# Kernel optimization log

Measured on AMD Instinct MI355X. Metric: run time of the kernel, lower is better.

The kernel has to match this reference:

```python
import jax, jax.numpy as jnp
import numpy as np

N, H = 65536, 256
RHO_REF = 1000.0
MOMENTUM_W, CONTINUITY_W = 1.0, 10.0


def setup_inputs() -> dict:
    key = jax.random.key(0)
    ks = jax.random.split(key, 6)
    sc = lambda k, shape, fan_in: jax.random.normal(k, shape, jnp.float32) * (1.0 / fan_in) ** 0.5
    return {
        "sample_points": jax.random.normal(ks[0], (N, 3), jnp.float32),
        "sample_times": jax.random.uniform(ks[1], (N, 1), jnp.float32),
        "viscosity": jax.random.uniform(ks[2], (N,), jnp.float32) * 1e-3 + 1e-6,
        "W1": sc(ks[3], (4, H), 4),
        "b1": jnp.zeros((H,), jnp.float32),
        "W2": sc(ks[4], (H, H), H),
        "b2": jnp.zeros((H,), jnp.float32),
        "W3": sc(ks[5], (H, 5), H),
        "b3": jnp.zeros((5,), jnp.float32),
    }


def reference(sample_points, sample_times, viscosity, W1, b1, W2, b2, W3, b3):
    gravity = jnp.array([0.0, -9.81, 0.0], dtype=sample_points.dtype)

    def mlp(z):  # z: (4,) = (x, y, zcoord, t) -> (5,) = (ux, uy, uz, p, rho_raw)
        h = jnp.tanh(z @ W1 + b1)
        h = jnp.tanh(h @ W2 + b2)
        return h @ W3 + b3

    def up_fn(z):  # (ux, uy, uz, p)
        return mlp(z)[:4]

    def u_fn(z):  # (ux, uy, uz)
        return mlp(z)[:3]

    def per_point(z):
        out = mlp(z)
        u = out[:3]
        rho = RHO_REF * (1.0 + 0.1 * jnp.tanh(out[4]))
        J = jax.jacfwd(up_fn)(z)                      # (4,4): d[u,p]/d[x,y,z,t]
        Hs = jax.jacfwd(jax.jacfwd(u_fn))(z)          # (3,4,4): second derivs of u
        lap = Hs[:, 0, 0] + Hs[:, 1, 1] + Hs[:, 2, 2]  # (3,) spatial Laplacian of u
        return u, rho, J, lap

    z = jnp.concatenate([sample_points, sample_times], axis=1)  # (N,4)
    u, rho, J, lap = jax.vmap(per_point)(z)

    du_dt = J[:, :3, 3]                                # (N,3)
    conv = jnp.einsum('nj,nij->ni', u, J[:, :3, :3])   # (u . grad) u
    grad_p = J[:, 3, :3]                               # (N,3)
    R = du_dt + conv + grad_p / rho[:, None] - viscosity[:, None] * lap - gravity[None, :]
    R_cont = J[:, 0, 0] + J[:, 1, 1] + J[:, 2, 2]      # div u

    momentum_loss = (R ** 2).mean(axis=0).sum()
    continuity_loss = (R_cont ** 2).mean()
    total = MOMENTUM_W * momentum_loss + CONTINUITY_W * continuity_loss
    return jnp.stack([total, momentum_loss, continuity_loss])
```

## Files before the change

kernel.cpp:

```cpp
#include <hip/hip_runtime.h>


#define NPTS 65536
#define TPB  8
#define NBLOCKS 256
#define TILES 32
#define KPAD 264
#define W3T_OFF 135168
#define PART_OFF 143360
#define TSZ 32768

typedef short s16x8 __attribute__((ext_vector_type(8)));
typedef float f32x4 __attribute__((ext_vector_type(4)));

static __device__ __forceinline__ unsigned short f2bf(float f){
  unsigned int u = __float_as_uint(f);
  u = (u + 0x7FFFu + ((u >> 16) & 1u)) >> 16;
  return (unsigned short)u;
}
static __device__ __forceinline__ unsigned cvtpk_bf16(float lo, float hi){
  unsigned r;
  asm("v_cvt_pk_bf16_f32 %0, %1, %2" : "=v"(r) : "v"(lo), "v"(hi));
  return r;
}
static __device__ __forceinline__ float fast_tanh(float x){
  float e = __builtin_amdgcn_exp2f(x * 2.8853900817779268f);
  return 1.f - 2.f * __builtin_amdgcn_rcpf(e + 1.f);
}

__global__ void prep_w2t(const float* __restrict__ W2, unsigned short* __restrict__ w2t){
  int k = blockIdx.x, j = threadIdx.x;
  w2t[j * KPAD + k] = f2bf(W2[k * 256 + j]);
}
__global__ void prep_w3t(const float* __restrict__ W3, unsigned short* __restrict__ w3t){
  int idx = blockIdx.x * 256 + threadIdx.x;
  int n = idx >> 8, k = idx & 255;
  w3t[n * 256 + k] = (n < 5) ? f2bf(W3[k * 5 + n]) : (unsigned short)0;
}

__launch_bounds__(512, 2)
__global__ void ns_main(const float* __restrict__ pts, const float* __restrict__ times,
                        const float* __restrict__ visc,
                        const float* __restrict__ W1, const float* __restrict__ b1,
                        const float* __restrict__ b2, const float* __restrict__ b3,
                        const unsigned short* __restrict__ w2t,
                        const unsigned short* __restrict__ w3t,
                        float* __restrict__ parts){
  __shared__ __align__(16) unsigned char sA[3 * TSZ];

  const int t   = threadIdx.x;
  const int blk = blockIdx.x;
  const int wid = t >> 6, lane = t & 63;
  const int g = lane >> 4, r16 = lane & 15;
  const int wr = wid >> 2, wc = wid & 3;
  const int xorv = (r16 & 7) << 4;

  const int p8 = t >> 6;
  const int jo = (t & 63) << 2;
  const float4 wa  = *(const float4*)(W1 + jo);
  const float4 wb  = *(const float4*)(W1 + 256 + jo);
  const float4 wc4 = *(const float4*)(W1 + 512 + jo);
  const float4 wd  = *(const float4*)(W1 + 768 + jo);
  const float4 bb  = *(const float4*)(b1 + jo);

  const unsigned char* w2tB = (const unsigned char*)w2t;
  const unsigned char* bp0 = w2tB + (((wc*64 +  0 + r16)*KPAD + g*8) << 1);
  const unsigned char* bp1 = w2tB + (((wc*64 + 16 + r16)*KPAD + g*8) << 1);
  const unsigned char* bp2 = w2tB + (((wc*64 + 32 + r16)*KPAD + g*8) << 1);
  const unsigned char* bp3 = w2tB + (((wc*64 + 48 + r16)*KPAD + g*8) << 1);
  float b2c[4];
  #pragma unroll
  for (int nt = 0; nt < 4; ++nt) b2c[nt] = b2[wc*64 + nt*16 + r16];
  const unsigned char* w3tB = (const unsigned char*)w3t + ((r16*256 + g*8) << 1);
  const float b3v = (r16 < 5) ? b3[r16] : 0.f;

  const int w3i = wid & 3;
  const int ptL = 2*w3i + ((r16 >> 2) & 1);
  const int jrow = ((ptL & 4) << 3) + ((ptL & 3) << 2) + (r16 & 3) + ((r16 >> 3) << 4);
  const int g3off = jrow * 512;
  const int g3sw  = (jrow & 7) << 4;

  float accM = 0.f, accC = 0.f;

  unsigned char *jA = sA, *jB = sA + TSZ, *jC = sA + 2*TSZ;

#define L1_TILE(NBASE, BASE) do {                                               \
    int n_ = (NBASE) + p8;                                                      \
    float z0_ = pts[n_*3+0], z1_ = pts[n_*3+1], z2_ = pts[n_*3+2], z3_ = times[n_]; \
    float th_[4], sg_[4], m2_[4];                                               \
    _Pragma("unroll")                                                           \
    for (int jj = 0; jj < 4; ++jj){                                             \
      float a_ = (&bb.x)[jj] + z0_*(&wa.x)[jj] + z1_*(&wb.x)[jj]                \
                             + z2_*(&wc4.x)[jj] + z3_*(&wd.x)[jj];              \
      float h_ = fast_tanh(a_);                                                 \
      th_[jj] = h_; sg_[jj] = 1.f - h_*h_; m2_[jj] = -2.f*h_*sg_[jj];           \
    }                                                                           \
    _Pragma("unroll")                                                           \
    for (int c = 0; c < 8; ++c){                                                \
      float x_[4];                                                              \
      _Pragma("unroll")                                                         \
      for (int jj = 0; jj < 4; ++jj){                                           \
        float w0_ = (&wa.x)[jj], w1_ = (&wb.x)[jj], w2_ = (&wc4.x)[jj];         \
        float v_;                                                               \
        if      (c == 0) v_ = th_[jj];                                          \
        else if (c == 1) v_ = sg_[jj]*w0_;                                      \
        else if (c == 2) v_ = sg_[jj]*w1_;                                      \
        else if (c == 3) v_ = sg_[jj]*w2_;                                      \
        else if (c == 4) v_ = sg_[jj]*(&wd.x)[jj];                              \
        else if (c == 5) v_ = m2_[jj]*w0_*w0_;                                  \
        else if (c == 6) v_ = m2_[jj]*w1_*w1_;                                  \
        else             v_ = m2_[jj]*w2_*w2_;                                  \
        x_[jj] = v_;                                                            \
      }                                                                         \
      int row_ = ((p8 & 4) << 3) + ((c & 4) << 2) + ((p8 & 3) << 2) + (c & 3);  \
      int off_ = row_*512 + (((jo << 1)) ^ ((row_ & 7) << 4));                  \
      uint2 v2_; v2_.x = cvtpk_bf16(x_[0], x_[1]); v2_.y = cvtpk_bf16(x_[2], x_[3]); \
      *(uint2*)((BASE) + off_) = v2_;                                           \
    }                                                                           \
  } while (0)

#define GEMM2_TILE(BASE, ACC) do {                                              \
    int abase_ = (wr*32 + r16)*512;                                             \
    s16x8 bc0_ = *(const s16x8*)(bp0), bc1_ = *(const s16x8*)(bp1);             \
    s16x8 bc2_ = *(const s16x8*)(bp2), bc3_ = *(const s16x8*)(bp3);             \
    _Pragma("unroll")                                                           \
    for (int ks = 0; ks < 8; ++ks){                                             \
      int X_ = ((ks*64) + (g << 4)) ^ xorv;                                     \
      s16x8 a0_ = *(const s16x8*)((BASE) + abase_ + X_);                        \
      s16x8 a1_ = *(const s16x8*)((BASE) + abase_ + 8192 + X_);                 \
      s16x8 bn0_, bn1_, bn2_, bn3_;                                             \
      if (ks < 7){                                                              \
        bn0_ = *(const s16x8*)(bp0 + (ks+1)*64);                                \
        bn1_ = *(const s16x8*)(bp1 + (ks+1)*64);                                \
        bn2_ = *(const s16x8*)(bp2 + (ks+1)*64);                                \
        bn3_ = *(const s16x8*)(bp3 + (ks+1)*64);                                \
      }                                                                         \
      __builtin_amdgcn_s_setprio(1);                                            \
      ACC[0][0] = __builtin_amdgcn_mfma_f32_16x16x32_bf16(a0_, bc0_, ACC[0][0], 0, 0, 0); \
      ACC[1][0] = __builtin_amdgcn_mfma_f32_16x16x32_bf16(a1_, bc0_, ACC[1][0], 0, 0, 0); \
      ACC[0][1] = __builtin_amdgcn_mfma_f32_16x16x32_bf16(a0_, bc1_, ACC[0][1], 0, 0, 0); \
      ACC[1][1] = __builtin_amdgcn_mfma_f32_16x16x32_bf16(a1_, bc1_, ACC[1][1], 0, 0, 0); \
      ACC[0][2] = __builtin_amdgcn_mfma_f32_16x16x32_bf16(a0_, bc2_, ACC[0][2], 0, 0, 0); \
      ACC[1][2] = __builtin_amdgcn_mfma_f32_16x16x32_bf16(a1_, bc2_, ACC[1][2], 0, 0, 0); \
      ACC[0][3] = __builtin_amdgcn_mfma_f32_16x16x32_bf16(a0_, bc3_, ACC[0][3], 0, 0, 0); \
      ACC[1][3] = __builtin_amdgcn_mfma_f32_16x16x32_bf16(a1_, bc3_, ACC[1][3], 0, 0, 0); \
      __builtin_amdgcn_s_setprio(0);                                            \
      bc0_ = bn0_; bc1_ = bn1_; bc2_ = bn2_; bc3_ = bn3_;                       \
    }                                                                           \
  } while (0)

#define RC_TILE(BASE, ACC) do {                                                 \
    _Pragma("unroll")                                                           \
    for (int nt = 0; nt < 4; ++nt){                                             \
      f32x4 v_ = ACC[0][nt];              \
      f32x4 w_ = ACC[1][nt];              \
      float gv_ = fast_tanh(v_[0] + b2c[nt]);                                   \
      float s2_ = 1.f - gv_*gv_;                                                \
      float t2_ = -2.f * gv_ * s2_;                                             \
      float r0_ = gv_,       r1_ = s2_*v_[1], r2_ = s2_*v_[2], r3_ = s2_*v_[3]; \
      float r4_ = s2_*w_[0];                                                    \
      float r5_ = fmaf(t2_*v_[1], v_[1], s2_*w_[1]);                            \
      float r6_ = fmaf(t2_*v_[2], v_[2], s2_*w_[2]);                            \
      float r7_ = fmaf(t2_*v_[3], v_[3], s2_*w_[3]);                            \
      int colb_ = (wc*64 + nt*16 + r16) << 1;                                   \
      int rb_   = (wr*32 + g*4)*512;                                            \
      unsigned u_;                                                              \
      u_ = cvtpk_bf16(r0_, r4_);                                                \
      *(unsigned short*)((BASE) + rb_        + (colb_ ^ ((((g&1)<<2)+0) << 4)))        = (unsigned short)u_; \
      *(unsigned short*)((BASE) + rb_        + (colb_ ^ ((((g&1)<<2)+0) << 4)) + 8192) = (unsigned short)(u_ >> 16); \
      u_ = cvtpk_bf16(r1_, r5_);                                                \
      *(unsigned short*)((BASE) + rb_ + 512  + (colb_ ^ ((((g&1)<<2)+1) << 4)))        = (unsigned short)u_; \
      *(unsigned short*)((BASE) + rb_ + 512  + (colb_ ^ ((((g&1)<<2)+1) << 4)) + 8192) = (unsigned short)(u_ >> 16); \
      u_ = cvtpk_bf16(r2_, r6_);                                                \
      *(unsigned short*)((BASE) + rb_ + 1024 + (colb_ ^ ((((g&1)<<2)+2) << 4)))        = (unsigned short)u_; \
      *(unsigned short*)((BASE) + rb_ + 1024 + (colb_ ^ ((((g&1)<<2)+2) << 4)) + 8192) = (unsigned short)(u_ >> 16); \
      u_ = cvtpk_bf16(r3_, r7_);                                                \
      *(unsigned short*)((BASE) + rb_ + 1536 + (colb_ ^ ((((g&1)<<2)+3) << 4)))        = (unsigned short)u_; \
      *(unsigned short*)((BASE) + rb_ + 1536 + (colb_ ^ ((((g&1)<<2)+3) << 4)) + 8192) = (unsigned short)(u_ >> 16); \
    }                                                                           \
  } while (0)

#define GEMM3_TAIL(BASE, NBASE) do {                                            \
    f32x4 a3_ = (f32x4){0.f, 0.f, 0.f, 0.f};                                    \
    _Pragma("unroll")                                                           \
    for (int ks = 0; ks < 8; ++ks){                                             \
      int X_ = ((ks*64) + (g << 4)) ^ g3sw;                                     \
      s16x8 av_ = *(const s16x8*)((BASE) + g3off + X_);                         \
      s16x8 bv_ = *(const s16x8*)(w3tB + ks*64);                                \
      a3_ = __builtin_amdgcn_mfma_f32_16x16x32_bf16(av_, bv_, a3_, 0, 0, 0);    \
    }                                                                           \
    float o4_ = __shfl_xor(a3_[0], 32, 64);                                     \
    float o5_ = __shfl_xor(a3_[1], 32, 64);                                     \
    float o6_ = __shfl_xor(a3_[2], 32, 64);                                     \
    float o7_ = __shfl_xor(a3_[3], 32, 64);                                     \
    float o0_ = a3_[0] + b3v, o1_ = a3_[1], o2_ = a3_[2], o3_ = a3_[3];         \
    int sl_ = lane & 16;                                                        \
    float u0_ = __shfl(o0_, sl_ | 0, 64);                                       \
    float u1_ = __shfl(o0_, sl_ | 1, 64);                                       \
    float u2_ = __shfl(o0_, sl_ | 2, 64);                                       \
    float rhoA_ = __shfl(o0_, sl_ | 4, 64);                                     \
    float gpx_ = __shfl(o1_, sl_ | 3, 64);                                      \
    float gpy_ = __shfl(o2_, sl_ | 3, 64);                                      \
    float gpz_ = __shfl(o3_, sl_ | 3, 64);                                      \
    float c00_ = __shfl(o1_, sl_ | 0, 64);                                      \
    float c11_ = __shfl(o2_, sl_ | 1, 64);                                      \
    float c22_ = __shfl(o3_, sl_ | 2, 64);                                      \
    float rho_ = 1000.f * (1.f + 0.1f * fast_tanh(rhoA_));                      \
    float rr_  = __builtin_amdgcn_rcpf(rho_);                                   \
    float vis_ = visc[(NBASE) + ptL];                                           \
    float lap_ = o5_ + o6_ + o7_;                                               \
    float cv_  = u0_*o1_ + u1_*o2_ + u2_*o3_;                                   \
    float gp_  = (r16 == 0) ? gpx_ : ((r16 == 1) ? gpy_ : gpz_);                \
    float R_   = o4_ + cv_ + gp_*rr_ - vis_*lap_ + ((r16 == 1) ? 9.81f : 0.f);  \
    if (lane < 32){                                                             \
      if (r16 < 3) accM += R_*R_;                                               \
      else if (r16 == 3){ float Rc_ = c00_ + c11_ + c22_; accC += Rc_*Rc_; }    \
    }                                                                           \
  } while (0)

  L1_TILE(blk*TILES*TPB, jA);
  __syncthreads();

  for (int i = 0; i < TILES; ++i){
    f32x4 acc[2][4];
    #pragma unroll
    for (int a = 0; a < 2; ++a)
      #pragma unroll
      for (int b = 0; b < 4; ++b)
        acc[a][b] = (f32x4){0.f, 0.f, 0.f, 0.f};
    GEMM2_TILE(jA, acc);
    if (i < TILES-1) L1_TILE((blk*TILES + i + 1)*TPB, jB);
    __syncthreads();

    RC_TILE(jA, acc);
    if (i > 0 && wid >= 4) GEMM3_TAIL(jC, (blk*TILES + i - 1)*TPB);
    __syncthreads();

    unsigned char* tmp = jA; jA = jB; jB = jC; jC = tmp;
  }
  if (wid >= 4) GEMM3_TAIL(jC, (blk*TILES + TILES - 1)*TPB);

  #pragma unroll
  for (int off = 1; off < 64; off <<= 1){
    accM += __shfl_xor(accM, off, 64);
    accC += __shfl_xor(accC, off, 64);
  }
  __syncthreads();
  float* red = (float*)sA;
  if (lane == 0){ red[wid*2] = accM; red[wid*2+1] = accC; }
  __syncthreads();
  if (t == 0){
    float m = 0.f, c = 0.f;
    #pragma unroll
    for (int w = 0; w < 8; ++w){ m += red[w*2]; c += red[w*2+1]; }
    float2 pr; pr.x = m; pr.y = c;
    *(float2*)(parts + blk*2) = pr;
  }
#undef L1_TILE
#undef GEMM2_TILE
#undef RC_TILE
#undef GEMM3_TAIL
}

__global__ void ns_reduce(const float* __restrict__ parts, float* __restrict__ out){
  int t = threadIdx.x;
  float a = 0.f, b = 0.f;
  if (t < NBLOCKS){ a = parts[2*t]; b = parts[2*t + 1]; }
  #pragma unroll
  for (int off = 32; off; off >>= 1){
    a += __shfl_down(a, off, 64);
    b += __shfl_down(b, off, 64);
  }
  __shared__ float sa[4], sb[4];
  int wid = t >> 6, lane = t & 63;
  if (lane == 0){ sa[wid] = a; sb[wid] = b; }
  __syncthreads();
  if (t == 0){
    float A = sa[0] + sa[1] + sa[2] + sa[3];
    float B = sb[0] + sb[1] + sb[2] + sb[3];
    float mom  = A / (float)NPTS;
    float cont = B / (float)NPTS;
    out[0] = mom + 10.f * cont;
    out[1] = mom;
    out[2] = cont;
  }
}

extern "C" void kernel_launch(void* const* d_in, const int* in_sizes, int n_in,
                              void* d_out, int out_size, void* d_ws, size_t ws_size,
                              hipStream_t stream) {
  const float* pts   = (const float*)d_in[0];
  const float* times = (const float*)d_in[1];
  const float* visc  = (const float*)d_in[2];
  const float* W1    = (const float*)d_in[3];
  const float* b1    = (const float*)d_in[4];
  const float* W2    = (const float*)d_in[5];
  const float* b2    = (const float*)d_in[6];
  const float* W3    = (const float*)d_in[7];
  const float* b3    = (const float*)d_in[8];
  float* out = (float*)d_out;

  unsigned short* w2t = (unsigned short*)d_ws;
  unsigned short* w3t = (unsigned short*)((char*)d_ws + W3T_OFF);
  float* parts        = (float*)((char*)d_ws + PART_OFF);

  prep_w2t<<<256, 256, 0, stream>>>(W2, w2t);
  prep_w3t<<<16, 256, 0, stream>>>(W3, w3t);
  ns_main<<<NBLOCKS, 512, 0, stream>>>(pts, times, visc, W1, b1, b2, b3, w2t, w3t, parts);
  ns_reduce<<<1, 256, 0, stream>>>(parts, out);
}
```

Measured before the change: 129.8 us.

## Split block into two staggered wave groups ping-ponging over separate LDS tiles

The 8 waves are split into two groups of 4. Each group owns its own pair of LDS tile buffers (LDS grows from 3 to 4 tiles) and processes alternate tiles. The groups run offset by one phase, so one group's MFMA GEMM2 overlaps the other's layer-1, tanh epilogue and GEMM3 work. Each wave now computes a full 64x64 output block (4x4 MFMA accumulators), and the B-fragment register prefetch is dropped. This trades more registers and LDS, plus two extra loop steps, for better overlap of matrix-core and vector work within a block.

After: 163.7 us. 26.1% more time.

```diff
diff --git a/kernel.cpp b/kernel.cpp
--- a/kernel.cpp
+++ b/kernel.cpp
@@ -46,17 +46,16 @@
                         const unsigned short* __restrict__ w2t,
                         const unsigned short* __restrict__ w3t,
                         float* __restrict__ parts){
-  __shared__ __align__(16) unsigned char sA[3 * TSZ];
+  __shared__ __align__(16) unsigned char sA[4 * TSZ];
 
   const int t   = threadIdx.x;
   const int blk = blockIdx.x;
   const int wid = t >> 6, lane = t & 63;
+  const int grp = wid >> 2, q = wid & 3;
   const int g = lane >> 4, r16 = lane & 15;
-  const int wr = wid >> 2, wc = wid & 3;
   const int xorv = (r16 & 7) << 4;
-
-  const int p8 = t >> 6;
-  const int jo = (t & 63) << 2;
+  const int jo = lane << 2;
+
   const float4 wa  = *(const float4*)(W1 + jo);
   const float4 wb  = *(const float4*)(W1 + 256 + jo);
   const float4 wc4 = *(const float4*)(W1 + 512 + jo);
@@ -64,123 +63,139 @@
   const float4 bb  = *(const float4*)(b1 + jo);
 
   const unsigned char* w2tB = (const unsigned char*)w2t;
-  const unsigned char* bp0 = w2tB + (((wc*64 +  0 + r16)*KPAD + g*8) << 1);
-  const unsigned char* bp1 = w2tB + (((wc*64 + 16 + r16)*KPAD + g*8) << 1);
-  const unsigned char* bp2 = w2tB + (((wc*64 + 32 + r16)*KPAD + g*8) << 1);
-  const unsigned char* bp3 = w2tB + (((wc*64 + 48 + r16)*KPAD + g*8) << 1);
+  const unsigned char* bp0 = w2tB + (((q*64 +  0 + r16)*KPAD + g*8) << 1);
+  const unsigned char* bp1 = w2tB + (((q*64 + 16 + r16)*KPAD + g*8) << 1);
+  const unsigned char* bp2 = w2tB + (((q*64 + 32 + r16)*KPAD + g*8) << 1);
+  const unsigned char* bp3 = w2tB + (((q*64 + 48 + r16)*KPAD + g*8) << 1);
   float b2c[4];
   #pragma unroll
-  for (int nt = 0; nt < 4; ++nt) b2c[nt] = b2[wc*64 + nt*16 + r16];
+  for (int nt = 0; nt < 4; ++nt) b2c[nt] = b2[q*64 + nt*16 + r16];
   const unsigned char* w3tB = (const unsigned char*)w3t + ((r16*256 + g*8) << 1);
   const float b3v = (r16 < 5) ? b3[r16] : 0.f;
 
-  const int w3i = wid & 3;
-  const int ptL = 2*w3i + ((r16 >> 2) & 1);
+  const int ptL  = 2*q + ((r16 >> 2) & 1);
   const int jrow = ((ptL & 4) << 3) + ((ptL & 3) << 2) + (r16 & 3) + ((r16 >> 3) << 4);
   const int g3off = jrow * 512;
   const int g3sw  = (jrow & 7) << 4;
 
+  const int tbase = blk * (TILES * TPB);
+
   float accM = 0.f, accC = 0.f;
-
-  unsigned char *jA = sA, *jB = sA + TSZ, *jC = sA + 2*TSZ;
-
-#define L1_TILE(NBASE, BASE) do {                                               \
-    int n_ = (NBASE) + p8;                                                      \
-    float z0_ = pts[n_*3+0], z1_ = pts[n_*3+1], z2_ = pts[n_*3+2], z3_ = times[n_]; \
-    float th_[4], sg_[4], m2_[4];                                               \
-    _Pragma("unroll")                                                           \
-    for (int jj = 0; jj < 4; ++jj){                                             \
-      float a_ = (&bb.x)[jj] + z0_*(&wa.x)[jj] + z1_*(&wb.x)[jj]                \
-                             + z2_*(&wc4.x)[jj] + z3_*(&wd.x)[jj];              \
-      float h_ = fast_tanh(a_);                                                 \
-      th_[jj] = h_; sg_[jj] = 1.f - h_*h_; m2_[jj] = -2.f*h_*sg_[jj];           \
-    }                                                                           \
-    _Pragma("unroll")                                                           \
-    for (int c = 0; c < 8; ++c){                                                \
-      float x_[4];                                                              \
+  f32x4 acc[4][4];
+
+#define L1_T(NBASE, BASE) do {                                                  \
+    _Pragma("unroll")                                                           \
+    for (int pp = 0; pp < 2; ++pp){                                             \
+      int p_ = 2*q + pp;                                                        \
+      int n_ = (NBASE) + p_;                                                    \
+      float z0_ = pts[n_*3+0], z1_ = pts[n_*3+1], z2_ = pts[n_*3+2], z3_ = times[n_]; \
+      float th_[4], sg_[4], m2_[4];                                             \
       _Pragma("unroll")                                                         \
       for (int jj = 0; jj < 4; ++jj){                                           \
-        float w0_ = (&wa.x)[jj], w1_ = (&wb.x)[jj], w2_ = (&wc4.x)[jj];         \
-        float v_;                                                               \
-        if      (c == 0) v_ = th_[jj];                                          \
-        else if (c == 1) v_ = sg_[jj]*w0_;                                      \
-        else if (c == 2) v_ = sg_[jj]*w1_;                                      \
-        else if (c == 3) v_ = sg_[jj]*w2_;                                      \
-        else if (c == 4) v_ = sg_[jj]*(&wd.x)[jj];                              \
-        else if (c == 5) v_ = m2_[jj]*w0_*w0_;                                  \
-        else if (c == 6) v_ = m2_[jj]*w1_*w1_;                                  \
-        else             v_ = m2_[jj]*w2_*w2_;                                  \
-        x_[jj] = v_;                                                            \
+        float a_ = (&bb.x)[jj] + z0_*(&wa.x)[jj] + z1_*(&wb.x)[jj]              \
+                               + z2_*(&wc4.x)[jj] + z3_*(&wd.x)[jj];            \
+        float h_ = fast_tanh(a_);                                               \
+        th_[jj] = h_; sg_[jj] = 1.f - h_*h_; m2_[jj] = -2.f*h_*sg_[jj];         \
       }                                                                         \
-      int row_ = ((p8 & 4) << 3) + ((c & 4) << 2) + ((p8 & 3) << 2) + (c & 3);  \
-      int off_ = row_*512 + (((jo << 1)) ^ ((row_ & 7) << 4));                  \
-      uint2 v2_; v2_.x = cvtpk_bf16(x_[0], x_[1]); v2_.y = cvtpk_bf16(x_[2], x_[3]); \
-      *(uint2*)((BASE) + off_) = v2_;                                           \
+      _Pragma("unroll")                                                         \
+      for (int c = 0; c < 8; ++c){                                              \
+        float x_[4];                                                            \
+        _Pragma("unroll")                                                       \
+        for (int jj = 0; jj < 4; ++jj){                                         \
+          float w0_ = (&wa.x)[jj], w1_ = (&wb.x)[jj], w2_ = (&wc4.x)[jj];       \
+          float v_;                                                             \
+          if      (c == 0) v_ = th_[jj];                                        \
+          else if (c == 1) v_ = sg_[jj]*w0_;                                    \
+          else if (c == 2) v_ = sg_[jj]*w1_;                                    \
+          else if (c == 3) v_ = sg_[jj]*w2_;                                    \
+          else if (c == 4) v_ = sg_[jj]*(&wd.x)[jj];                            \
+          else if (c == 5) v_ = m2_[jj]*w0_*w0_;                                \
+          else if (c == 6) v_ = m2_[jj]*w1_*w1_;                                \
+          else             v_ = m2_[jj]*w2_*w2_;                                \
+          x_[jj] = v_;                                                          \
+        }                                                                       \
+        int row_ = ((p_ & 4) << 3) + ((c & 4) << 2) + ((p_ & 3) << 2) + (c & 3);\
+        int off_ = row_*512 + ((jo << 1) ^ ((row_ & 7) << 4));                  \
+        uint2 v2_; v2_.x = cvtpk_bf16(x_[0], x_[1]); v2_.y = cvtpk_bf16(x_[2], x_[3]); \
+        *(uint2*)((BASE) + off_) = v2_;                                         \
+      }                                                                         \
     }                                                                           \
   } while (0)
 
-#define GEMM2_TILE(BASE, ACC) do {                                              \
-    int abase_ = (wr*32 + r16)*512;                                             \
-    s16x8 bc0_ = *(const s16x8*)(bp0), bc1_ = *(const s16x8*)(bp1);             \
-    s16x8 bc2_ = *(const s16x8*)(bp2), bc3_ = *(const s16x8*)(bp3);             \
+#define G2_T(BASE) do {                                                         \
+    _Pragma("unroll")                                                           \
+    for (int a_ = 0; a_ < 4; ++a_)                                              \
+      _Pragma("unroll")                                                         \
+      for (int b_ = 0; b_ < 4; ++b_)                                            \
+        acc[a_][b_] = (f32x4){0.f, 0.f, 0.f, 0.f};                              \
+    int abase_ = r16*512;                                                       \
     _Pragma("unroll")                                                           \
     for (int ks = 0; ks < 8; ++ks){                                             \
       int X_ = ((ks*64) + (g << 4)) ^ xorv;                                     \
-      s16x8 a0_ = *(const s16x8*)((BASE) + abase_ + X_);                        \
-      s16x8 a1_ = *(const s16x8*)((BASE) + abase_ + 8192 + X_);                 \
-      s16x8 bn0_, bn1_, bn2_, bn3_;                                             \
-      if (ks < 7){                                                              \
-        bn0_ = *(const s16x8*)(bp0 + (ks+1)*64);                                \
-        bn1_ = *(const s16x8*)(bp1 + (ks+1)*64);                                \
-        bn2_ = *(const s16x8*)(bp2 + (ks+1)*64);                                \
-        bn3_ = *(const s16x8*)(bp3 + (ks+1)*64);                                \
+      s16x8 af0_ = *(const s16x8*)((BASE) + abase_ + X_);                       \
+      s16x8 af1_ = *(const s16x8*)((BASE) + abase_ +  8192 + X_);               \
+      s16x8 af2_ = *(const s16x8*)((BASE) + abase_ + 16384 + X_);               \
+      s16x8 af3_ = *(const s16x8*)((BASE) + abase_ + 24576 + X_);               \
+      s16x8 b0_ = *(const s16x8*)(bp0 + ks*64);                                 \
+      s16x8 b1_ = *(const s16x8*)(bp1 + ks*64);                                 \
+      s16x8 b2_ = *(const s16x8*)(bp2 + ks*64);                                 \
+      s16x8 b3_ = *(const s16x8*)(bp3 + ks*64);                                 \
+      __builtin_amdgcn_s_setprio(1);                                            \
+      acc[0][0] = __builtin_amdgcn_mfma_f32_16x16x32_bf16(af0_, b0_, acc[0][0], 0, 0, 0); \
+      acc[1][0] = __builtin_amdgcn_mfma_f32_16x16x32_bf16(af1_, b0_, acc[1][0], 0, 0, 0); \
+      acc[2][0] = __builtin_amdgcn_mfma_f32_16x16x32_bf16(af2_, b0_, acc[2][0], 0, 0, 0); \
+      acc[3][0] = __builtin_amdgcn_mfma_f32_16x16x32_bf16(af3_, b0_, acc[3][0], 0, 0, 0); \
+      acc[0][1] = __builtin_amdgcn_mfma_f32_16x16x32_bf16(af0_, b1_, acc[0][1], 0, 0, 0); \
+      acc[1][1] = __builtin_amdgcn_mfma_f32_16x16x32_bf16(af1_, b1_, acc[1][1], 0, 0, 0); \
+      acc[2][1] = __builtin_amdgcn_mfma_f32_16x16x32_bf16(af2_, b1_, acc[2][1], 0, 0, 0); \
+      acc[3][1] = __builtin_amdgcn_mfma_f32_16x16x32_bf16(af3_, b1_, acc[3][1], 0, 0, 0); \
+      acc[0][2] = __builtin_amdgcn_mfma_f32_16x16x32_bf16(af0_, b2_, acc[0][2], 0, 0, 0); \
+      acc[1][2] = __builtin_amdgcn_mfma_f32_16x16x32_bf16(af1_, b2_, acc[1][2], 0, 0, 0); \
+      acc[2][2] = __builtin_amdgcn_mfma_f32_16x16x32_bf16(af2_, b2_, acc[2][2], 0, 0, 0); \
+      acc[3][2] = __builtin_amdgcn_mfma_f32_16x16x32_bf16(af3_, b2_, acc[3][2], 0, 0, 0); \
+      acc[0][3] = __builtin_amdgcn_mfma_f32_16x16x32_bf16(af0_, b3_, acc[0][3], 0, 0, 0); \
+      acc[1][3] = __builtin_amdgcn_mfma_f32_16x16x32_bf16(af1_, b3_, acc[1][3], 0, 0, 0); \
+      acc[2][3] = __builtin_amdgcn_mfma_f32_16x16x32_bf16(af2_, b3_, acc[2][3], 0, 0, 0); \
+      acc[3][3] = __builtin_amdgcn_mfma_f32_16x16x32_bf16(af3_, b3_, acc[3][3], 0, 0, 0); \
+      __builtin_amdgcn_s_setprio(0);                                            \
+    }                                                                           \
+  } while (0)
+
+#define RC_T(BASE) do {                                                         \
+    _Pragma("unroll")                                                           \
+    for (int pr = 0; pr < 2; ++pr){                                             \
+      _Pragma("unroll")                                                         \
+      for (int nt = 0; nt < 4; ++nt){                                           \
+        f32x4 v_ = acc[2*pr][nt];                                               \
+        f32x4 w_ = acc[2*pr+1][nt];                                             \
+        float gv_ = fast_tanh(v_[0] + b2c[nt]);                                 \
+        float s2_ = 1.f - gv_*gv_;                                              \
+        float t2_ = -2.f * gv_ * s2_;                                           \
+        float r0_ = gv_,       r1_ = s2_*v_[1], r2_ = s2_*v_[2], r3_ = s2_*v_[3]; \
+        float r4_ = s2_*w_[0];                                                  \
+        float r5_ = fmaf(t2_*v_[1], v_[1], s2_*w_[1]);                          \
+        float r6_ = fmaf(t2_*v_[2], v_[2], s2_*w_[2]);                          \
+        float r7_ = fmaf(t2_*v_[3], v_[3], s2_*w_[3]);                          \
+        int colb_ = (q*64 + nt*16 + r16) << 1;                                  \
+        int rb_   = pr*16384 + (g*4)*512;                                       \
+        unsigned u_;                                                            \
+        u_ = cvtpk_bf16(r0_, r4_);                                              \
+        *(unsigned short*)((BASE) + rb_        + (colb_ ^ ((((g&1)<<2)+0) << 4)))        = (unsigned short)u_; \
+        *(unsigned short*)((BASE) + rb_        + (colb_ ^ ((((g&1)<<2)+0) << 4)) + 8192) = (unsigned short)(u_ >> 16); \
+        u_ = cvtpk_bf16(r1_, r5_);                                              \
+        *(unsigned short*)((BASE) + rb_ + 512  + (colb_ ^ ((((g&1)<<2)+1) << 4)))        = (unsigned short)u_; \
+        *(unsigned short*)((BASE) + rb_ + 512  + (colb_ ^ ((((g&1)<<2)+1) << 4)) + 8192) = (unsigned short)(u_ >> 16); \
+        u_ = cvtpk_bf16(r2_, r6_);                                              \
+        *(unsigned short*)((BASE) + rb_ + 1024 + (colb_ ^ ((((g&1)<<2)+2) << 4)))        = (unsigned short)u_; \
+        *(unsigned short*)((BASE) + rb_ + 1024 + (colb_ ^ ((((g&1)<<2)+2) << 4)) + 8192) = (unsigned short)(u_ >> 16); \
+        u_ = cvtpk_bf16(r3_, r7_);                                              \
+        *(unsigned short*)((BASE) + rb_ + 1536 + (colb_ ^ ((((g&1)<<2)+3) << 4)))        = (unsigned short)u_; \
+        *(unsigned short*)((BASE) + rb_ + 1536 + (colb_ ^ ((((g&1)<<2)+3) << 4)) + 8192) = (unsigned short)(u_ >> 16); \
       }                                                                         \
-      __builtin_amdgcn_s_setprio(1);                                            \
-      ACC[0][0] = __builtin_amdgcn_mfma_f32_16x16x32_bf16(a0_, bc0_, ACC[0][0], 0, 0, 0); \
-      ACC[1][0] = __builtin_amdgcn_mfma_f32_16x16x32_bf16(a1_, bc0_, ACC[1][0], 0, 0, 0); \
-      ACC[0][1] = __builtin_amdgcn_mfma_f32_16x16x32_bf16(a0_, bc1_, ACC[0][1], 0, 0, 0); \
-      ACC[1][1] = __builtin_amdgcn_mfma_f32_16x16x32_bf16(a1_, bc1_, ACC[1][1], 0, 0, 0); \
-      ACC[0][2] = __builtin_amdgcn_mfma_f32_16x16x32_bf16(a0_, bc2_, ACC[0][2], 0, 0, 0); \
-      ACC[1][2] = __builtin_amdgcn_mfma_f32_16x16x32_bf16(a1_, bc2_, ACC[1][2], 0, 0, 0); \
-      ACC[0][3] = __builtin_amdgcn_mfma_f32_16x16x32_bf16(a0_, bc3_, ACC[0][3], 0, 0, 0); \
-      ACC[1][3] = __builtin_amdgcn_mfma_f32_16x16x32_bf16(a1_, bc3_, ACC[1][3], 0, 0, 0); \
-      __builtin_amdgcn_s_setprio(0);                                            \
-      bc0_ = bn0_; bc1_ = bn1_; bc2_ = bn2_; bc3_ = bn3_;                       \
     }                                                                           \
   } while (0)
 
-#define RC_TILE(BASE, ACC) do {                                                 \
-    _Pragma("unroll")                                                           \
-    for (int nt = 0; nt < 4; ++nt){                                             \
-      f32x4 v_ = ACC[0][nt];              \
-      f32x4 w_ = ACC[1][nt];              \
-      float gv_ = fast_tanh(v_[0] + b2c[nt]);                                   \
-      float s2_ = 1.f - gv_*gv_;                                                \
-      float t2_ = -2.f * gv_ * s2_;                                             \
-      float r0_ = gv_,       r1_ = s2_*v_[1], r2_ = s2_*v_[2], r3_ = s2_*v_[3]; \
-      float r4_ = s2_*w_[0];                                                    \
-      float r5_ = fmaf(t2_*v_[1], v_[1], s2_*w_[1]);                            \
-      float r6_ = fmaf(t2_*v_[2], v_[2], s2_*w_[2]);                            \
-      float r7_ = fmaf(t2_*v_[3], v_[3], s2_*w_[3]);                            \
-      int colb_ = (wc*64 + nt*16 + r16) << 1;                                   \
-      int rb_   = (wr*32 + g*4)*512;                                            \
-      unsigned u_;                                                              \
-      u_ = cvtpk_bf16(r0_, r4_);                                                \
-      *(unsigned short*)((BASE) + rb_        + (colb_ ^ ((((g&1)<<2)+0) << 4)))        = (unsigned short)u_; \
-      *(unsigned short*)((BASE) + rb_        + (colb_ ^ ((((g&1)<<2)+0) << 4)) + 8192) = (unsigned short)(u_ >> 16); \
-      u_ = cvtpk_bf16(r1_, r5_);                                                \
-      *(unsigned short*)((BASE) + rb_ + 512  + (colb_ ^ ((((g&1)<<2)+1) << 4)))        = (unsigned short)u_; \
-      *(unsigned short*)((BASE) + rb_ + 512  + (colb_ ^ ((((g&1)<<2)+1) << 4)) + 8192) = (unsigned short)(u_ >> 16); \
-      u_ = cvtpk_bf16(r2_, r6_);                                                \
-      *(unsigned short*)((BASE) + rb_ + 1024 + (colb_ ^ ((((g&1)<<2)+2) << 4)))        = (unsigned short)u_; \
-      *(unsigned short*)((BASE) + rb_ + 1024 + (colb_ ^ ((((g&1)<<2)+2) << 4)) + 8192) = (unsigned short)(u_ >> 16); \
-      u_ = cvtpk_bf16(r3_, r7_);                                                \
-      *(unsigned short*)((BASE) + rb_ + 1536 + (colb_ ^ ((((g&1)<<2)+3) << 4)))        = (unsigned short)u_; \
-      *(unsigned short*)((BASE) + rb_ + 1536 + (colb_ ^ ((((g&1)<<2)+3) << 4)) + 8192) = (unsigned short)(u_ >> 16); \
-    }                                                                           \
-  } while (0)
-
-#define GEMM3_TAIL(BASE, NBASE) do {                                            \
+#define G3_T(BASE, NBASE) do {                                                  \
     f32x4 a3_ = (f32x4){0.f, 0.f, 0.f, 0.f};                                    \
     _Pragma("unroll")                                                           \
     for (int ks = 0; ks < 8; ++ks){                                             \
@@ -218,34 +233,30 @@
     }                                                                           \
   } while (0)
 
-  L1_TILE(blk*TILES*TPB, jA);
-  __syncthreads();
-
-  for (int i = 0; i < TILES; ++i){
-    f32x4 acc[2][4];
-    #pragma unroll
-    for (int a = 0; a < 2; ++a)
-      #pragma unroll
-      for (int b = 0; b < 4; ++b)
-        acc[a][b] = (f32x4){0.f, 0.f, 0.f, 0.f};
-    GEMM2_TILE(jA, acc);
-    if (i < TILES-1) L1_TILE((blk*TILES + i + 1)*TPB, jB);
+  #pragma unroll 1
+  for (int k = 0; k <= 34; ++k){
+    int a = k - grp;
+    if (a == 0){
+      L1_T(tbase + grp*TPB, sA + (grp << 1)*TSZ);
+    } else if (a > 0 && a <= 33){
+      if (a & 1){
+        int j = (a - 1) >> 1;
+        if (j > 0)  G3_T(sA + ((grp << 1) | ((j-1) & 1))*TSZ, tbase + (2*(j-1)+grp)*TPB);
+        if (j < 16) G2_T(sA + ((grp << 1) | (j & 1))*TSZ);
+      } else {
+        int j = (a - 2) >> 1;
+        RC_T(sA + ((grp << 1) | (j & 1))*TSZ);
+        if (j < 15) L1_T(tbase + (2*(j+1)+grp)*TPB, sA + ((grp << 1) | ((j+1) & 1))*TSZ);
+      }
+    }
     __syncthreads();
-
-    RC_TILE(jA, acc);
-    if (i > 0 && wid >= 4) GEMM3_TAIL(jC, (blk*TILES + i - 1)*TPB);
-    __syncthreads();
-
-    unsigned char* tmp = jA; jA = jB; jB = jC; jC = tmp;
-  }
-  if (wid >= 4) GEMM3_TAIL(jC, (blk*TILES + TILES - 1)*TPB);
+  }
 
   #pragma unroll
   for (int off = 1; off < 64; off <<= 1){
     accM += __shfl_xor(accM, off, 64);
     accC += __shfl_xor(accC, off, 64);
   }
-  __syncthreads();
   float* red = (float*)sA;
   if (lane == 0){ red[wid*2] = accM; red[wid*2+1] = accC; }
   __syncthreads();
@@ -256,10 +267,10 @@
     float2 pr; pr.x = m; pr.y = c;
     *(float2*)(parts + blk*2) = pr;
   }
-#undef L1_TILE
-#undef GEMM2_TILE
-#undef RC_TILE
-#undef GEMM3_TAIL
+#undef L1_T
+#undef G2_T
+#undef RC_T
+#undef G3_T
 }
 
 __global__ void ns_reduce(const float* __restrict__ parts, float* __restrict__ out){
```
